# Kernel optimization log

Hardware: AMD Instinct MI355X
Metric: run time of the kernel (lower is better)

## Reference

```python
import jax, jax.numpy as jnp
import numpy as np

EMB = 1024
HEADS = 16
HEAD_SIZE = EMB // HEADS


def setup_inputs() -> dict:
    key = jax.random.key(0)
    ks = jax.random.split(key, 10)
    s = 1.0 / np.sqrt(EMB)
    return {
        "x": jax.random.normal(ks[0], (2, 2048, EMB), dtype=jnp.float32),
        "ln_gamma": jnp.ones((EMB,), jnp.float32),
        "ln_beta": jnp.zeros((EMB,), jnp.float32),
        "Wq": jax.random.normal(ks[1], (EMB, EMB), jnp.float32) * s,
        "bq": jnp.zeros((EMB,), jnp.float32),
        "Wk": jax.random.normal(ks[2], (EMB, EMB), jnp.float32) * s,
        "bk": jnp.zeros((EMB,), jnp.float32),
        "Wv": jax.random.normal(ks[3], (EMB, EMB), jnp.float32) * s,
        "bv": jnp.zeros((EMB,), jnp.float32),
        "Wo": jax.random.normal(ks[4], (EMB, EMB), jnp.float32) * s,
        "bo": jnpps if False else jnp.zeros((EMB,), jnp.float32),
    }


def _layernorm(x, gamma, beta, eps=1e-5):
    mu = jnp.mean(x, axis=-1, keepdims=True)
    var = jnp.mean(jnp.square(x - mu), axis=-1, keepdims=True)
    return (x - mu) * jax.lax.rsqrt(var + eps) * gamma + beta


def reference(x, ln_gamma, ln_beta, Wq, bq, Wk, bk, Wv, bv, Wo, bo):
    B, L, D = x.shape
    h = _layernorm(x, ln_gamma, ln_beta)
    # projections -> [B, H, L, hd]
    def split_heads(t):
        return t.reshape(B, L, HEADS, HEAD_SIZE).transpose(0, 2, 1, 3)
    q = split_heads(h @ Wq.T + bq)
    k = split_heads(h @ Wk.T + bk)
    v = split_heads(h @ Wv.T + bv)
    scale = HEAD_SIZE ** (-0.5)
    w = jnp.einsum("bhqd,bhkd->bhqk", q, k) * scale  # [B,H,L,L]
    w = jax.nn.softmax(w, axis=-1)
    o = jnp.einsum("bhqk,bhkd->bhqd", w, v)
    o = o.transpose(0, 2, 1, 3).reshape(B, L, D)
    o = o @ Wo.T + bo
    return x + o
```

## Files before the change

### kernel.cpp

```cpp
#include <hip/hip_runtime.h>
#include <math.h>

#define B_   2
#define L_   2048
#define EMB_ 1024
#define H_   16
#define HD_  64
#define M_   (B_ * L_)
#define KSPLIT 4
#define LOG2E 1.44269504088896f

typedef __bf16 bf16x8 __attribute__((ext_vector_type(8)));
typedef __bf16 bf16x4 __attribute__((ext_vector_type(4)));
typedef __bf16 bf16x2 __attribute__((ext_vector_type(2)));
typedef float floatx16 __attribute__((ext_vector_type(16)));

typedef __attribute__((address_space(1))) const void GV;
typedef __attribute__((address_space(3))) void LV;

#define MFMA32(a, b, c) __builtin_amdgcn_mfma_f32_32x32x16_bf16((a), (b), (c), 0, 0, 0)

#if __has_builtin(__builtin_amdgcn_exp2f)
#define EXP2(x) __builtin_amdgcn_exp2f(x)
#else
#define EXP2(x) exp2f(x)
#endif

#define SWZ(row) ((((row) & 7) ^ (((row) >> 3) & 3)))

__device__ __forceinline__ int pkbf(float a, float b) {
#if __has_builtin(__builtin_amdgcn_cvt_pk_bf16_f32)
    union { bf16x2 v; int i; } u;
    u.v = __builtin_amdgcn_cvt_pk_bf16_f32(a, b);
    return u.i;
#else
    union { __bf16 h[2]; int i; } u;
    u.h[0] = (__bf16)a; u.h[1] = (__bf16)b;
    return u.i;
#endif
}

__global__ __launch_bounds__(256) void cvt_w_kernel(
        const float* __restrict__ s0, const float* __restrict__ s1,
        const float* __restrict__ s2, const float* __restrict__ s3,
        __bf16* __restrict__ d0, __bf16* __restrict__ d1,
        __bf16* __restrict__ d2, __bf16* __restrict__ d3) {
    int z = blockIdx.y;
    const float* s = (z == 0) ? s0 : (z == 1) ? s1 : (z == 2) ? s2 : s3;
    __bf16* d = (z == 0) ? d0 : (z == 1) ? d1 : (z == 2) ? d2 : d3;
    size_t base = (size_t)(blockIdx.x * 256 + threadIdx.x) * 16;
#pragma unroll
    for (int j = 0; j < 4; ++j) {
        float4 f = *(const float4*)(s + base + j * 4);
        bf16x4 t;
        t[0] = (__bf16)f.x; t[1] = (__bf16)f.y; t[2] = (__bf16)f.z; t[3] = (__bf16)f.w;
        *(bf16x4*)(d + base + j * 4) = t;
    }
}

__global__ __launch_bounds__(256) void ln_kernel(
        const float* __restrict__ x, const float* __restrict__ gamma,
        const float* __restrict__ beta, __bf16* __restrict__ h) {
    int row = blockIdx.x;
    int tid = threadIdx.x;
    const float* xr = x + (size_t)row * EMB_;
    float4 v = *(const float4*)(xr + tid * 4);
    float s  = v.x + v.y + v.z + v.w;
    float ss = v.x * v.x + v.y * v.y + v.z * v.z + v.w * v.w;
    for (int off = 32; off; off >>= 1) {
        s  += __shfl_down(s, off, 64);
        ss += __shfl_down(ss, off, 64);
    }
    __shared__ float s1[4], s2[4];
    int wid = tid >> 6;
    if ((tid & 63) == 0) { s1[wid] = s; s2[wid] = ss; }
    __syncthreads();
    if (tid == 0) {
        float a = s1[0] + s1[1] + s1[2] + s1[3];
        float b = s2[0] + s2[1] + s2[2] + s2[3];
        float mu = a / EMB_;
        float var = b / EMB_ - mu * mu;
        s1[0] = mu;
        s2[0] = rsqrtf(var + 1e-5f);
    }
    __syncthreads();
    float mu = s1[0], rstd = s2[0];
    float4 g4 = *(const float4*)(gamma + tid * 4);
    float4 b4 = *(const float4*)(beta + tid * 4);
    bf16x4 o;
    o[0] = (__bf16)((v.x - mu) * rstd * g4.x + b4.x);
    o[1] = (__bf16)((v.y - mu) * rstd * g4.y + b4.y);
    o[2] = (__bf16)((v.z - mu) * rstd * g4.z + b4.z);
    o[3] = (__bf16)((v.w - mu) * rstd * g4.w + b4.w);
    *(bf16x4*)(h + (size_t)row * EMB_ + tid * 4) = o;
}

template <int SEGS>
__device__ __forceinline__ void stage_tile(const __bf16* gbase, __bf16* lds,
                                           int wave, int lane) {
    int srow = lane >> 3;
    int gch0 = lane & 7;
#pragma unroll
    for (int s = 0; s < SEGS; ++s) {
        int seg = wave * SEGS + s;
        int row = seg * 8 + srow;
        int g = gch0 ^ SWZ(row);
        __builtin_amdgcn_global_load_lds(
            (GV*)(gbase + (size_t)row * EMB_ + g * 8),
            (LV*)(lds + seg * 512 + lane * 8), 16, 0, 0);
    }
}

__global__ __launch_bounds__(256) void gemm_qkv_mfma(
        const __bf16* __restrict__ A,
        const __bf16* __restrict__ Wqb, const __bf16* __restrict__ Wkb,
        const __bf16* __restrict__ Wvb,
        const float* __restrict__ bq, const float* __restrict__ bk,
        const float* __restrict__ bv,
        __bf16* __restrict__ Qo, __bf16* __restrict__ Ko,
        __bf16* __restrict__ Vto) {
    __shared__ __bf16 As[64 * 64];
    __shared__ __bf16 Bs[128 * 64];
    const int z = blockIdx.z;
    const __bf16* W = (z == 0) ? Wqb : (z == 1) ? Wkb : Wvb;
    const float* bias = (z == 0) ? bq : (z == 1) ? bk : bv;

    int tid = threadIdx.x, wave = tid >> 6, lane = tid & 63;
    int quad = lane >> 5, lq = lane & 31;
    int bm = blockIdx.y * 64, bn = blockIdx.x * 128;

    floatx16 acc[2];
#pragma unroll
    for (int i = 0; i < 2; ++i)
#pragma unroll
        for (int r = 0; r < 16; ++r) acc[i][r] = 0.f;

    for (int k0 = 0; k0 < EMB_; k0 += 64) {
        __syncthreads();
        stage_tile<2>(A + (size_t)bm * EMB_ + k0, As, wave, lane);
        stage_tile<4>(W + (size_t)bn * EMB_ + k0, Bs, wave, lane);
        __syncthreads();
#pragma unroll
        for (int s = 0; s < 4; ++s) {
            int g = 2 * s + quad;
            int r0 = lq, r1 = lq + 32;
            int c = wave * 32 + lq;
            bf16x8 a0 = *(const bf16x8*)&As[r0 * 64 + ((g ^ SWZ(r0)) * 8)];
            bf16x8 a1 = *(const bf16x8*)&As[r1 * 64 + ((g ^ SWZ(r1)) * 8)];
            bf16x8 b  = *(const bf16x8*)&Bs[c * 64 + ((g ^ SWZ(c)) * 8)];
            acc[0] = MFMA32(a0, b, acc[0]);
            acc[1] = MFMA32(a1, b, acc[1]);
        }
    }

    float qscale = (z == 0) ? 0.125f * LOG2E : 1.0f;
    int col = bn + wave * 32 + lq;
    float bv_ = bias[col];
#pragma unroll
    for (int mb = 0; mb < 2; ++mb) {
        if (z < 2) {
            __bf16* dst = (z == 0) ? Qo : Ko;
#pragma unroll
            for (int r = 0; r < 16; ++r) {
                int row = bm + mb * 32 + (r & 3) + 8 * (r >> 2) + 4 * quad;
                dst[(size_t)row * EMB_ + col] = (__bf16)((acc[mb][r] + bv_) * qscale);
            }
        } else {
            int hh = col >> 6, d = col & 63;
#pragma unroll
            for (int rb = 0; rb < 4; ++rb) {
                int row = bm + mb * 32 + 8 * rb + 4 * quad;
                int b = row >> 11, l = row & (L_ - 1);
                bf16x4 t;
#pragma unroll
                for (int a = 0; a < 4; ++a) t[a] = (__bf16)(acc[mb][4 * rb + a] + bv_);
                *(bf16x4*)(Vto + ((size_t)(b * H_ + hh) * HD_ + d) * L_ + l) = t;
            }
        }
    }
}

__global__ __launch_bounds__(256) void gemm_out_mfma(
        const __bf16* __restrict__ A, const __bf16* __restrict__ W,
        const float* __restrict__ bias, const float* __restrict__ x,
        float* __restrict__ out) {
    __shared__ __bf16 As[64 * 64];
    __shared__ __bf16 Bs[128 * 64];
    int tid = threadIdx.x, wave = tid >> 6, lane = tid & 63;
    int quad = lane >> 5, lq = lane & 31;
    int bm = blockIdx.y * 64, bn = blockIdx.x * 128;

    floatx16 acc[2];
#pragma unroll
    for (int i = 0; i < 2; ++i)
#pragma unroll
        for (int r = 0; r < 16; ++r) acc[i][r] = 0.f;

    for (int k0 = 0; k0 < EMB_; k0 += 64) {
        __syncthreads();
        stage_tile<2>(A + (size_t)bm * EMB_ + k0, As, wave, lane);
        stage_tile<4>(W + (size_t)bn * EMB_ + k0, Bs, wave, lane);
        __syncthreads();
#pragma unroll
        for (int s = 0; s < 4; ++s) {
            int g = 2 * s + quad;
            int r0 = lq, r1 = lq + 32;
            int c = wave * 32 + lq;
            bf16x8 a0 = *(const bf16x8*)&As[r0 * 64 + ((g ^ SWZ(r0)) * 8)];
            bf16x8 a1 = *(const bf16x8*)&As[r1 * 64 + ((g ^ SWZ(r1)) * 8)];
            bf16x8 b  = *(const bf16x8*)&Bs[c * 64 + ((g ^ SWZ(c)) * 8)];
            acc[0] = MFMA32(a0, b, acc[0]);
            acc[1] = MFMA32(a1, b, acc[1]);
        }
    }

    int col = bn + wave * 32 + lq;
    float bv_ = bias[col];
#pragma unroll
    for (int mb = 0; mb < 2; ++mb) {
#pragma unroll
        for (int r = 0; r < 16; ++r) {
            size_t row = bm + mb * 32 + (r & 3) + 8 * (r >> 2) + 4 * quad;
            out[row * EMB_ + col] = acc[mb][r] + bv_ + x[row * EMB_ + col];
        }
    }
}

__global__ __launch_bounds__(64) void attn_mfma(
        const __bf16* __restrict__ Q,
        const __bf16* __restrict__ K,
        const __bf16* __restrict__ Vt,
        __bf16* __restrict__ Op,
        float* __restrict__ Lp) {
    int lane = threadIdx.x;
    int quad = lane >> 5, lq = lane & 31;
    int bh = blockIdx.x;
    int ks = blockIdx.z;
    int b = bh >> 4, h = bh & 15;
    int q0 = blockIdx.y * 64;
    const size_t tok0 = (size_t)b * L_;

    const __bf16* Kb = K + tok0 * EMB_ + h * HD_;
    const __bf16* Vb = Vt + (size_t)bh * HD_ * L_;

    bf16x8 qf[2][4];
#pragma unroll
    for (int qb = 0; qb < 2; ++qb) {
        const __bf16* qp = Q + (tok0 + q0 + qb * 32 + lq) * EMB_ + h * HD_ + quad * 8;
#pragma unroll
        for (int s = 0; s < 4; ++s) qf[qb][s] = *(const bf16x8*)(qp + s * 16);
    }

    floatx16 oacc[2][2];
#pragma unroll
    for (int i = 0; i < 2; ++i)
#pragma unroll
        for (int j = 0; j < 2; ++j)
#pragma unroll
            for (int r = 0; r < 16; ++r) oacc[i][j][r] = 0.f;
    float lacc[2] = {0.f, 0.f};

    auto loadKV = [&](int kt, bf16x8 kf[4], bf16x8 vf[2][2]) {
#pragma unroll
        for (int s = 0; s < 4; ++s)
            kf[s] = *(const bf16x8*)(Kb + (size_t)(kt + lq) * EMB_ + s * 16 + quad * 8);
#pragma unroll
        for (int kst = 0; kst < 2; ++kst)
#pragma unroll
            for (int db = 0; db < 2; ++db)
                vf[kst][db] = *(const bf16x8*)(Vb + (size_t)(db * 32 + lq) * L_ +
                                               kt + kst * 16 + quad * 8);
    };

    auto computeStep = [&](const bf16x8 kf[4], const bf16x8 vf[2][2]) {
#pragma unroll
        for (int qb = 0; qb < 2; ++qb) {
            floatx16 sacc;
#pragma unroll
            for (int r = 0; r < 16; ++r) sacc[r] = 0.f;
#pragma unroll
            for (int s = 0; s < 4; ++s) sacc = MFMA32(kf[s], qf[qb][s], sacc);

            int P[8];
            float lsum = 0.f;
#pragma unroll
            for (int t = 0; t < 8; ++t) {
                float pa = EXP2(sacc[2 * t]);
                float pb = EXP2(sacc[2 * t + 1]);
                lsum += pa + pb;
                P[t] = pkbf(pa, pb);
            }
            lacc[qb] += lsum;
            int X[8];
#pragma unroll
            for (int t = 0; t < 8; ++t) X[t] = __shfl_xor(P[t], 32, 64);
            union { int i[4]; bf16x8 v; } bf0, bf1;
            bf0.i[0] = quad ? X[2] : P[0];
            bf0.i[1] = quad ? X[3] : P[1];
            bf0.i[2] = quad ? P[2] : X[0];
            bf0.i[3] = quad ? P[3] : X[1];
            bf1.i[0] = quad ? X[6] : P[4];
            bf1.i[1] = quad ? X[7] : P[5];
            bf1.i[2] = quad ? P[6] : X[4];
            bf1.i[3] = quad ? P[7] : X[5];
#pragma unroll
            for (int db = 0; db < 2; ++db) {
                oacc[qb][db] = MFMA32(vf[0][db], bf0.v, oacc[qb][db]);
                oacc[qb][db] = MFMA32(vf[1][db], bf1.v, oacc[qb][db]);
            }
        }
    };

    const int kt0 = ks * (L_ / KSPLIT);
    const int kt1 = kt0 + L_ / KSPLIT;

    bf16x8 kfA[4], vfA[2][2], kfB[4], vfB[2][2];
    loadKV(kt0, kfA, vfA);
    for (int kt = kt0; kt < kt1; kt += 64) {
        loadKV(kt + 32, kfB, vfB);
        computeStep(kfA, vfA);
        int ktn = (kt + 64 < kt1) ? kt + 64 : kt0;
        loadKV(ktn, kfA, vfA);
        computeStep(kfB, vfB);
    }

#pragma unroll
    for (int qb = 0; qb < 2; ++qb) {
        float l = lacc[qb] + __shfl_xor(lacc[qb], 32, 64);
        if (lane < 32)
            Lp[((size_t)ks * 32 + bh) * L_ + q0 + qb * 32 + lane] = l;
    }
#pragma unroll
    for (int qb = 0; qb < 2; ++qb)
#pragma unroll
        for (int db = 0; db < 2; ++db)
#pragma unroll
            for (int r = 0; r < 16; ++r) {
                int dp = db * 32 + (r & 3) + 8 * (r >> 2) + 4 * quad;
                Op[((size_t)(ks * 32 + bh) * HD_ + dp) * L_ + q0 + qb * 32 + lq] =
                    (__bf16)oacc[qb][db][r];
            }
}

__global__ __launch_bounds__(256) void combine_kernel(
        const __bf16* __restrict__ Op, const float* __restrict__ Lp,
        __bf16* __restrict__ Ob) {
    __shared__ float lrl[64];
    __shared__ __bf16 T[64][72];
    int t = threadIdx.x;
    int qt = blockIdx.x * 64;
    int bh = blockIdx.y;
    int b = bh >> 4, h = bh & 15;

    if (t < 64) {
        float l = 0.f;
#pragma unroll
        for (int ks = 0; ks < KSPLIT; ++ks)
            l += Lp[((size_t)ks * 32 + bh) * L_ + qt + t];
        lrl[t] = 1.0f / l;
    }
    __syncthreads();

#pragma unroll
    for (int cc = 0; cc < 2; ++cc) {
        int id = t + cc * 256;
        int d = id >> 3, q8 = (id & 7) * 8;
        float acc[8];
#pragma unroll
        for (int j = 0; j < 8; ++j) acc[j] = 0.f;
#pragma unroll
        for (int ks = 0; ks < KSPLIT; ++ks) {
            bf16x8 v = *(const bf16x8*)(Op + ((size_t)(ks * 32 + bh) * HD_ + d) * L_ + qt + q8);
#pragma unroll
            for (int j = 0; j < 8; ++j) acc[j] += (float)v[j];
        }
#pragma unroll
        for (int j = 0; j < 8; ++j)
            T[q8 + j][d] = (__bf16)(acc[j] * lrl[q8 + j]);
    }
    __syncthreads();

#pragma unroll
    for (int cc = 0; cc < 2; ++cc) {
        int id = t + cc * 256;
        int tl = id >> 3, dc = (id & 7) * 8;
        bf16x8 v = *(const bf16x8*)&T[tl][dc];
        *(bf16x8*)(Ob + ((size_t)b * L_ + qt + tl) * EMB_ + h * HD_ + dc) = v;
    }
}

extern "C" void kernel_launch(void* const* d_in, const int* in_sizes, int n_in,
                              void* d_out, int out_size, void* d_ws, size_t ws_size,
                              hipStream_t stream) {
    const float* x     = (const float*)d_in[0];
    const float* gamma = (const float*)d_in[1];
    const float* beta  = (const float*)d_in[2];
    const float* Wq    = (const float*)d_in[3];
    const float* bq    = (const float*)d_in[4];
    const float* Wk    = (const float*)d_in[5];
    const float* bk    = (const float*)d_in[6];
    const float* Wv    = (const float*)d_in[7];
    const float* bv    = (const float*)d_in[8];
    const float* Wo    = (const float*)d_in[9];
    const float* bo    = (const float*)d_in[10];
    float* out = (float*)d_out;

    const size_t SLAB = (size_t)M_ * EMB_;
    const size_t WSLAB = (size_t)EMB_ * EMB_;
    char* ws = (char*)d_ws;
    __bf16* hb   = (__bf16*)ws;                       ws += SLAB * 2;
    __bf16* Qb   = (__bf16*)ws;                       ws += SLAB * 2;
    __bf16* Kb   = (__bf16*)ws;                       ws += SLAB * 2;
    __bf16* Vtb  = (__bf16*)ws;                       ws += SLAB * 2;
    __bf16* Wqb  = (__bf16*)ws;                       ws += WSLAB * 2;
    __bf16* Wkb  = (__bf16*)ws;                       ws += WSLAB * 2;
    __bf16* Wvb  = (__bf16*)ws;                       ws += WSLAB * 2;
    __bf16* Wob  = (__bf16*)ws;                       ws += WSLAB * 2;
    __bf16* Op   = (__bf16*)ws;                       ws += (size_t)KSPLIT * SLAB * 2;
    float*  Lp   = (float*)ws;                        ws += (size_t)KSPLIT * 32 * L_ * 4;
    __bf16* Ob   = hb;

    cvt_w_kernel<<<dim3(256, 4), 256, 0, stream>>>(Wq, Wk, Wv, Wo, Wqb, Wkb, Wvb, Wob);
    ln_kernel<<<M_, 256, 0, stream>>>(x, gamma, beta, hb);
    gemm_qkv_mfma<<<dim3(EMB_ / 128, M_ / 64, 3), 256, 0, stream>>>(
        hb, Wqb, Wkb, Wvb, bq, bk, bv, Qb, Kb, Vtb);
    attn_mfma<<<dim3(B_ * H_, L_ / 64, KSPLIT), 64, 0, stream>>>(Qb, Kb, Vtb, Op, Lp);
    combine_kernel<<<dim3(L_ / 64, B_ * H_), 256, 0, stream>>>(Op, Lp, Ob);
    gemm_out_mfma<<<dim3(EMB_ / 128, M_ / 64), 256, 0, stream>>>(Ob, Wob, bo, x, out);
}
```

Before: 233.6 us.

## Share K/V tiles via LDS across four attention waves and enlarge QKV GEMM tiles

The attention kernel moves from one wave per block loading K/V straight from global memory into registers, to four waves per block. Each block stages 64-key K and V^T tiles into double-buffered, swizzled LDS with global_load_lds, and all four query sub-tiles reuse those tiles. The QKV projection becomes one GEMM over a concatenated weight buffer with 128x128 tiles and a 2x2 wave layout, replacing three launches' worth of z-split 64x128 tiles. This cuts redundant global K/V traffic and raises per-wave MFMA reuse, at the cost of more LDS use and a barrier per key tile.

```diff
diff --git a/kernel.cpp b/kernel.cpp
--- a/kernel.cpp
+++ b/kernel.cpp
@@ -95,6 +95,95 @@
     *(bf16x4*)(h + (size_t)row * EMB_ + tid * 4) = o;
 }
 
+__device__ __forceinline__ void stage_tile128(const __bf16* gbase, __bf16* lds,
+                                              int wave, int lane) {
+    int srow = lane >> 3;
+    int gch0 = lane & 7;
+#pragma unroll
+    for (int s = 0; s < 4; ++s) {
+        int seg = wave * 4 + s;
+        int row = seg * 8 + srow;
+        int g = gch0 ^ SWZ(row);
+        __builtin_amdgcn_global_load_lds(
+            (GV*)(gbase + (size_t)row * EMB_ + g * 8),
+            (LV*)(lds + seg * 512 + lane * 8), 16, 0, 0);
+    }
+}
+
+__global__ __launch_bounds__(256) void gemm_qkv_mfma(
+        const __bf16* __restrict__ A, const __bf16* __restrict__ W,
+        const float* __restrict__ bq, const float* __restrict__ bk,
+        const float* __restrict__ bv,
+        __bf16* __restrict__ Qo, __bf16* __restrict__ Ko,
+        __bf16* __restrict__ Vto) {
+    __shared__ __bf16 As[128 * 64];
+    __shared__ __bf16 Bs[128 * 64];
+    int tid = threadIdx.x, wave = tid >> 6, lane = tid & 63;
+    int wm = wave >> 1, wn = wave & 1;
+    int quad = lane >> 5, lq = lane & 31;
+    int bm = blockIdx.y * 128, bn = blockIdx.x * 128;
+
+    floatx16 acc[2][2];
+#pragma unroll
+    for (int i = 0; i < 2; ++i)
+#pragma unroll
+        for (int j = 0; j < 2; ++j)
+#pragma unroll
+            for (int r = 0; r < 16; ++r) acc[i][j][r] = 0.f;
+
+    for (int k0 = 0; k0 < EMB_; k0 += 64) {
+        __syncthreads();
+        stage_tile128(A + (size_t)bm * EMB_ + k0, As, wave, lane);
+        stage_tile128(W + (size_t)bn * EMB_ + k0, Bs, wave, lane);
+        __syncthreads();
+#pragma unroll
+        for (int s = 0; s < 4; ++s) {
+            int g = 2 * s + quad;
+            int r0 = wm * 64 + lq, r1 = r0 + 32;
+            int c0 = wn * 64 + lq, c1 = c0 + 32;
+            bf16x8 a0 = *(const bf16x8*)&As[r0 * 64 + ((g ^ SWZ(r0)) * 8)];
+            bf16x8 a1 = *(const bf16x8*)&As[r1 * 64 + ((g ^ SWZ(r1)) * 8)];
+            bf16x8 b0 = *(const bf16x8*)&Bs[c0 * 64 + ((g ^ SWZ(c0)) * 8)];
+            bf16x8 b1 = *(const bf16x8*)&Bs[c1 * 64 + ((g ^ SWZ(c1)) * 8)];
+            acc[0][0] = MFMA32(a0, b0, acc[0][0]);
+            acc[0][1] = MFMA32(a0, b1, acc[0][1]);
+            acc[1][0] = MFMA32(a1, b0, acc[1][0]);
+            acc[1][1] = MFMA32(a1, b1, acc[1][1]);
+        }
+    }
+
+#pragma unroll
+    for (int mb = 0; mb < 2; ++mb) {
+#pragma unroll
+        for (int nb = 0; nb < 2; ++nb) {
+            int col = bn + wn * 64 + nb * 32 + lq;
+            int z = col >> 10;
+            int cc = col & 1023;
+            float bv_ = (z == 0) ? bq[cc] : (z == 1) ? bk[cc] : bv[cc];
+            if (z < 2) {
+                __bf16* dst = (z == 0) ? Qo : Ko;
+                float qs = (z == 0) ? 0.125f * LOG2E : 1.0f;
+#pragma unroll
+                for (int r = 0; r < 16; ++r) {
+                    int row = bm + wm * 64 + mb * 32 + (r & 3) + 8 * (r >> 2) + 4 * quad;
+                    dst[(size_t)row * EMB_ + cc] = (__bf16)((acc[mb][nb][r] + bv_) * qs);
+                }
+            } else {
+                int hh = cc >> 6, d = cc & 63;
+#pragma unroll
+                for (int rb = 0; rb < 4; ++rb) {
+                    int row = bm + wm * 64 + mb * 32 + 8 * rb + 4 * quad;
+                    int b = row >> 11, l = row & (L_ - 1);
+                    bf16x4 t;
+#pragma unroll
+                    for (int a = 0; a < 4; ++a) t[a] = (__bf16)(acc[mb][nb][4 * rb + a] + bv_);
+                    *(bf16x4*)(Vto + ((size_t)(b * H_ + hh) * HD_ + d) * L_ + l) = t;
+                }
+            }
+        }
+    }
+}
+
 template <int SEGS>
 __device__ __forceinline__ void stage_tile(const __bf16* gbase, __bf16* lds,
                                            int wave, int lane) {
@@ -111,20 +200,12 @@
     }
 }
 
-__global__ __launch_bounds__(256) void gemm_qkv_mfma(
-        const __bf16* __restrict__ A,
-        const __bf16* __restrict__ Wqb, const __bf16* __restrict__ Wkb,
-        const __bf16* __restrict__ Wvb,
-        const float* __restrict__ bq, const float* __restrict__ bk,
-        const float* __restrict__ bv,
-        __bf16* __restrict__ Qo, __bf16* __restrict__ Ko,
-        __bf16* __restrict__ Vto) {
+__global__ __launch_bounds__(256) void gemm_out_mfma(
+        const __bf16* __restrict__ A, const __bf16* __restrict__ W,
+        const float* __restrict__ bias, const float* __restrict__ x,
+        float* __restrict__ out) {
     __shared__ __bf16 As[64 * 64];
     __shared__ __bf16 Bs[128 * 64];
-    const int z = blockIdx.z;
-    const __bf16* W = (z == 0) ? Wqb : (z == 1) ? Wkb : Wvb;
-    const float* bias = (z == 0) ? bq : (z == 1) ? bk : bv;
-
     int tid = threadIdx.x, wave = tid >> 6, lane = tid & 63;
     int quad = lane >> 5, lq = lane & 31;
     int bm = blockIdx.y * 64, bn = blockIdx.x * 128;
@@ -153,67 +234,6 @@
         }
     }
 
-    float qscale = (z == 0) ? 0.125f * LOG2E : 1.0f;
-    int col = bn + wave * 32 + lq;
-    float bv_ = bias[col];
-#pragma unroll
-    for (int mb = 0; mb < 2; ++mb) {
-        if (z < 2) {
-            __bf16* dst = (z == 0) ? Qo : Ko;
-#pragma unroll
-            for (int r = 0; r < 16; ++r) {
-                int row = bm + mb * 32 + (r & 3) + 8 * (r >> 2) + 4 * quad;
-                dst[(size_t)row * EMB_ + col] = (__bf16)((acc[mb][r] + bv_) * qscale);
-            }
-        } else {
-            int hh = col >> 6, d = col & 63;
-#pragma unroll
-            for (int rb = 0; rb < 4; ++rb) {
-                int row = bm + mb * 32 + 8 * rb + 4 * quad;
-                int b = row >> 11, l = row & (L_ - 1);
-                bf16x4 t;
-#pragma unroll
-                for (int a = 0; a < 4; ++a) t[a] = (__bf16)(acc[mb][4 * rb + a] + bv_);
-                *(bf16x4*)(Vto + ((size_t)(b * H_ + hh) * HD_ + d) * L_ + l) = t;
-            }
-        }
-    }
-}
-
-__global__ __launch_bounds__(256) void gemm_out_mfma(
-        const __bf16* __restrict__ A, const __bf16* __restrict__ W,
-        const float* __restrict__ bias, const float* __restrict__ x,
-        float* __restrict__ out) {
-    __shared__ __bf16 As[64 * 64];
-    __shared__ __bf16 Bs[128 * 64];
-    int tid = threadIdx.x, wave = tid >> 6, lane = tid & 63;
-    int quad = lane >> 5, lq = lane & 31;
-    int bm = blockIdx.y * 64, bn = blockIdx.x * 128;
-
-    floatx16 acc[2];
-#pragma unroll
-    for (int i = 0; i < 2; ++i)
-#pragma unroll
-        for (int r = 0; r < 16; ++r) acc[i][r] = 0.f;
-
-    for (int k0 = 0; k0 < EMB_; k0 += 64) {
-        __syncthreads();
-        stage_tile<2>(A + (size_t)bm * EMB_ + k0, As, wave, lane);
-        stage_tile<4>(W + (size_t)bn * EMB_ + k0, Bs, wave, lane);
-        __syncthreads();
-#pragma unroll
-        for (int s = 0; s < 4; ++s) {
-            int g = 2 * s + quad;
-            int r0 = lq, r1 = lq + 32;
-            int c = wave * 32 + lq;
-            bf16x8 a0 = *(const bf16x8*)&As[r0 * 64 + ((g ^ SWZ(r0)) * 8)];
-            bf16x8 a1 = *(const bf16x8*)&As[r1 * 64 + ((g ^ SWZ(r1)) * 8)];
-            bf16x8 b  = *(const bf16x8*)&Bs[c * 64 + ((g ^ SWZ(c)) * 8)];
-            acc[0] = MFMA32(a0, b, acc[0]);
-            acc[1] = MFMA32(a1, b, acc[1]);
-        }
-    }
-
     int col = bn + wave * 32 + lq;
     float bv_ = bias[col];
 #pragma unroll
@@ -226,18 +246,21 @@
     }
 }
 
-__global__ __launch_bounds__(64) void attn_mfma(
+__global__ __launch_bounds__(256) void attn_mfma(
         const __bf16* __restrict__ Q,
         const __bf16* __restrict__ K,
         const __bf16* __restrict__ Vt,
         __bf16* __restrict__ Op,
         float* __restrict__ Lp) {
-    int lane = threadIdx.x;
+    __shared__ __bf16 Ks[2][64 * 64];
+    __shared__ __bf16 Vs[2][64 * 64];
+
+    int tid = threadIdx.x, wave = tid >> 6, lane = tid & 63;
     int quad = lane >> 5, lq = lane & 31;
     int bh = blockIdx.x;
     int ks = blockIdx.z;
     int b = bh >> 4, h = bh & 15;
-    int q0 = blockIdx.y * 64;
+    int q0 = blockIdx.y * 256 + wave * 64;
     const size_t tok0 = (size_t)b * L_;
 
     const __bf16* Kb = K + tok0 * EMB_ + h * HD_;
@@ -260,68 +283,88 @@
             for (int r = 0; r < 16; ++r) oacc[i][j][r] = 0.f;
     float lacc[2] = {0.f, 0.f};
 
-    auto loadKV = [&](int kt, bf16x8 kf[4], bf16x8 vf[2][2]) {
-#pragma unroll
-        for (int s = 0; s < 4; ++s)
-            kf[s] = *(const bf16x8*)(Kb + (size_t)(kt + lq) * EMB_ + s * 16 + quad * 8);
-#pragma unroll
-        for (int kst = 0; kst < 2; ++kst)
-#pragma unroll
-            for (int db = 0; db < 2; ++db)
-                vf[kst][db] = *(const bf16x8*)(Vb + (size_t)(db * 32 + lq) * L_ +
-                                               kt + kst * 16 + quad * 8);
+    int srow = lane >> 3, gch0 = lane & 7;
+
+    auto stage = [&](int buf, int kt) {
+#pragma unroll
+        for (int s = 0; s < 2; ++s) {
+            int seg = wave * 2 + s;
+            int row = seg * 8 + srow;
+            int g = gch0 ^ SWZ(row);
+            __builtin_amdgcn_global_load_lds(
+                (GV*)(Kb + (size_t)(kt + row) * EMB_ + g * 8),
+                (LV*)(&Ks[buf][seg * 512 + lane * 8]), 16, 0, 0);
+            __builtin_amdgcn_global_load_lds(
+                (GV*)(Vb + (size_t)row * L_ + kt + g * 8),
+                (LV*)(&Vs[buf][seg * 512 + lane * 8]), 16, 0, 0);
+        }
     };
 
-    auto computeStep = [&](const bf16x8 kf[4], const bf16x8 vf[2][2]) {
-#pragma unroll
-        for (int qb = 0; qb < 2; ++qb) {
-            floatx16 sacc;
-#pragma unroll
-            for (int r = 0; r < 16; ++r) sacc[r] = 0.f;
-#pragma unroll
-            for (int s = 0; s < 4; ++s) sacc = MFMA32(kf[s], qf[qb][s], sacc);
-
-            int P[8];
-            float lsum = 0.f;
-#pragma unroll
-            for (int t = 0; t < 8; ++t) {
-                float pa = EXP2(sacc[2 * t]);
-                float pb = EXP2(sacc[2 * t + 1]);
-                lsum += pa + pb;
-                P[t] = pkbf(pa, pb);
+    auto compute = [&](int buf) {
+#pragma unroll
+        for (int nb = 0; nb < 2; ++nb) {
+            int krow = nb * 32 + lq;
+            bf16x8 kf[4];
+#pragma unroll
+            for (int s = 0; s < 4; ++s)
+                kf[s] = *(const bf16x8*)&Ks[buf][krow * 64 + (((2 * s + quad) ^ SWZ(krow)) * 8)];
+            bf16x8 vf[2][2];
+#pragma unroll
+            for (int half = 0; half < 2; ++half) {
+                int t = 2 * nb + half;
+#pragma unroll
+                for (int db = 0; db < 2; ++db) {
+                    int drow = db * 32 + lq;
+                    vf[half][db] = *(const bf16x8*)&Vs[buf][drow * 64 + (((2 * t + quad) ^ SWZ(drow)) * 8)];
+                }
             }
-            lacc[qb] += lsum;
-            int X[8];
-#pragma unroll
-            for (int t = 0; t < 8; ++t) X[t] = __shfl_xor(P[t], 32, 64);
-            union { int i[4]; bf16x8 v; } bf0, bf1;
-            bf0.i[0] = quad ? X[2] : P[0];
-            bf0.i[1] = quad ? X[3] : P[1];
-            bf0.i[2] = quad ? P[2] : X[0];
-            bf0.i[3] = quad ? P[3] : X[1];
-            bf1.i[0] = quad ? X[6] : P[4];
-            bf1.i[1] = quad ? X[7] : P[5];
-            bf1.i[2] = quad ? P[6] : X[4];
-            bf1.i[3] = quad ? P[7] : X[5];
-#pragma unroll
-            for (int db = 0; db < 2; ++db) {
-                oacc[qb][db] = MFMA32(vf[0][db], bf0.v, oacc[qb][db]);
-                oacc[qb][db] = MFMA32(vf[1][db], bf1.v, oacc[qb][db]);
+#pragma unroll
+            for (int qb = 0; qb < 2; ++qb) {
+                floatx16 sacc;
+#pragma unroll
+                for (int r = 0; r < 16; ++r) sacc[r] = 0.f;
+#pragma unroll
+                for (int s = 0; s < 4; ++s) sacc = MFMA32(kf[s], qf[qb][s], sacc);
+
+                int P[8];
+                float lsum = 0.f;
+#pragma unroll
+                for (int t = 0; t < 8; ++t) {
+                    float pa = EXP2(sacc[2 * t]);
+                    float pb = EXP2(sacc[2 * t + 1]);
+                    lsum += pa + pb;
+                    P[t] = pkbf(pa, pb);
+                }
+                lacc[qb] += lsum;
+                int X[8];
+#pragma unroll
+                for (int t = 0; t < 8; ++t) X[t] = __shfl_xor(P[t], 32, 64);
+                union { int i[4]; bf16x8 v; } bf0, bf1;
+                bf0.i[0] = quad ? X[2] : P[0];
+                bf0.i[1] = quad ? X[3] : P[1];
+                bf0.i[2] = quad ? P[2] : X[0];
+                bf0.i[3] = quad ? P[3] : X[1];
+                bf1.i[0] = quad ? X[6] : P[4];
+                bf1.i[1] = quad ? X[7] : P[5];
+                bf1.i[2] = quad ? P[6] : X[4];
+                bf1.i[3] = quad ? P[7] : X[5];
+#pragma unroll
+                for (int db = 0; db < 2; ++db) {
+                    oacc[qb][db] = MFMA32(vf[0][db], bf0.v, oacc[qb][db]);
+                    oacc[qb][db] = MFMA32(vf[1][db], bf1.v, oacc[qb][db]);
+                }
             }
         }
     };
 
     const int kt0 = ks * (L_ / KSPLIT);
-    const int kt1 = kt0 + L_ / KSPLIT;
-
-    bf16x8 kfA[4], vfA[2][2], kfB[4], vfB[2][2];
-    loadKV(kt0, kfA, vfA);
-    for (int kt = kt0; kt < kt1; kt += 64) {
-        loadKV(kt + 32, kfB, vfB);
-        computeStep(kfA, vfA);
-        int ktn = (kt + 64 < kt1) ? kt + 64 : kt0;
-        loadKV(ktn, kfA, vfA);
-        computeStep(kfB, vfB);
+    const int NT = (L_ / KSPLIT) / 64;
+
+    stage(0, kt0);
+    for (int t = 0; t < NT; ++t) {
+        __syncthreads();
+        if (t + 1 < NT) stage((t + 1) & 1, kt0 + (t + 1) * 64);
+        compute(t & 1);
     }
 
 #pragma unroll
@@ -408,23 +451,22 @@
     const size_t SLAB = (size_t)M_ * EMB_;
     const size_t WSLAB = (size_t)EMB_ * EMB_;
     char* ws = (char*)d_ws;
-    __bf16* hb   = (__bf16*)ws;                       ws += SLAB * 2;
-    __bf16* Qb   = (__bf16*)ws;                       ws += SLAB * 2;
-    __bf16* Kb   = (__bf16*)ws;                       ws += SLAB * 2;
-    __bf16* Vtb  = (__bf16*)ws;                       ws += SLAB * 2;
-    __bf16* Wqb  = (__bf16*)ws;                       ws += WSLAB * 2;
-    __bf16* Wkb  = (__bf16*)ws;                       ws += WSLAB * 2;
-    __bf16* Wvb  = (__bf16*)ws;                       ws += WSLAB * 2;
-    __bf16* Wob  = (__bf16*)ws;                       ws += WSLAB * 2;
-    __bf16* Op   = (__bf16*)ws;                       ws += (size_t)KSPLIT * SLAB * 2;
-    float*  Lp   = (float*)ws;                        ws += (size_t)KSPLIT * 32 * L_ * 4;
-    __bf16* Ob   = hb;
-
-    cvt_w_kernel<<<dim3(256, 4), 256, 0, stream>>>(Wq, Wk, Wv, Wo, Wqb, Wkb, Wvb, Wob);
+    __bf16* hb    = (__bf16*)ws;                      ws += SLAB * 2;
+    __bf16* Qb    = (__bf16*)ws;                      ws += SLAB * 2;
+    __bf16* Kb    = (__bf16*)ws;                      ws += SLAB * 2;
+    __bf16* Vtb   = (__bf16*)ws;                      ws += SLAB * 2;
+    __bf16* Wqkvb = (__bf16*)ws;                      ws += 3 * WSLAB * 2;
+    __bf16* Wob   = (__bf16*)ws;                      ws += WSLAB * 2;
+    __bf16* Op    = (__bf16*)ws;                      ws += (size_t)KSPLIT * SLAB * 2;
+    float*  Lp    = (float*)ws;                       ws += (size_t)KSPLIT * 32 * L_ * 4;
+    __bf16* Ob    = hb;
+
+    cvt_w_kernel<<<dim3(256, 4), 256, 0, stream>>>(
+        Wq, Wk, Wv, Wo, Wqkvb, Wqkvb + WSLAB, Wqkvb + 2 * WSLAB, Wob);
     ln_kernel<<<M_, 256, 0, stream>>>(x, gamma, beta, hb);
-    gemm_qkv_mfma<<<dim3(EMB_ / 128, M_ / 64, 3), 256, 0, stream>>>(
-        hb, Wqb, Wkb, Wvb, bq, bk, bv, Qb, Kb, Vtb);
-    attn_mfma<<<dim3(B_ * H_, L_ / 64, KSPLIT), 64, 0, stream>>>(Qb, Kb, Vtb, Op, Lp);
+    gemm_qkv_mfma<<<dim3(3 * EMB_ / 128, M_ / 128), 256, 0, stream>>>(
+        hb, Wqkvb, bq, bk, bv, Qb, Kb, Vtb);
+    attn_mfma<<<dim3(B_ * H_, L_ / 256, KSPLIT), 256, 0, stream>>>(Qb, Kb, Vtb, Op, Lp);
     combine_kernel<<<dim3(L_ / 64, B_ * H_), 256, 0, stream>>>(Op, Lp, Ob);
     gemm_out_mfma<<<dim3(EMB_ / 128, M_ / 64), 256, 0, stream>>>(Ob, Wob, bo, x, out);
 }
```

Result: no change. 236.0 us (+1.0%).
